# Performance work log

Hardware: AMD Instinct MI355X
Metric: run time of the kernel (lower is better)

Reference implementation:

```python
import jax, jax.numpy as jnp
import numpy as np

B, P, IN, OUT = 32, 128, 64, 32

def _logm(S):
    # symmetric PD matrix log via eigh: U diag(log w) U^T
    w, U = jnp.linalg.eigh(S)
    return jnp.einsum('...ij,...j,...kj->...ik', U, jnp.log(w), U)

def _expm(S):
    w, U = jnp.linalg.eigh(S)
    return jnp.einsum('...ij,...j,...kj->...ik', U, jnp.exp(w), U)

def setup_inputs() -> dict:
    key = jax.random.key(0)
    k1, k2, k3, k4 = jax.random.split(key, 4)
    # SPD input: A A^T / n + eps I
    A = jax.random.normal(k1, (B, P, IN, IN), dtype=jnp.float32)
    x = A @ jnp.swapaxes(A, -1, -2) / IN + 1e-3 * jnp.eye(IN, dtype=jnp.float32)
    scale = 1.0 / np.sqrt(IN)
    Wq = jax.random.normal(k2, (OUT, IN), dtype=jnp.float32) * scale
    Wk = jax.random.normal(k3, (OUT, IN), dtype=jnp.float32) * scale
    Wv = jax.random.normal(k4, (OUT, IN), dtype=jnp.float32) * scale
    return {"x": x, "Wq": Wq, "Wk": Wk, "Wv": Wv}

def reference(x, Wq, Wk, Wv):
    def bimap(W, S):  # W S W^T, keeps SPD
        return jnp.einsum('oi,bpij,kj->bpok', W, S, W)
    Q = bimap(Wq, x)   # (B,P,OUT,OUT)
    K = bimap(Wk, x)
    V = bimap(Wv, x)
    LQ, LK, LV = _logm(Q), _logm(K), _logm(V)
    # log-Euclidean squared distance d_ij = ||log Qi - log Kj||_F^2
    qq = jnp.sum(LQ * LQ, axis=(-2, -1))          # (B,P)
    kk = jnp.sum(LK * LK, axis=(-2, -1))          # (B,P)
    qk = jnp.einsum('bpij,bqij->bpq', LQ, LK)     # (B,P,P)
    energy = jnp.maximum(qq[:, :, None] + kk[:, None, :] - 2.0 * qk, 0.0)
    weights = 1.0 / (1.0 + jnp.log1p(energy))     # (B,Pq,Pk)
    prob = jax.nn.softmax(weights, axis=-2)       # softmax over query axis (dim=-2)
    prob = jnp.transpose(prob, (0, 2, 1))         # (B,P,P)
    # weighted Frechet (log-Euclidean) mean: exp(sum_j w_ij log V_j)
    mean_log = jnp.einsum('bij,bjkl->bikl', prob, LV)  # (B,P,OUT,OUT)
    return _expm(mean_log)
```

## Files before the change

kernel.cpp:

```cpp
#include <hip/hip_runtime.h>
#include <math.h>

#define NB   32
#define NP   128
#define NM   4096
#define NMAT3 12288

typedef float v2f __attribute__((ext_vector_type(2)));

#if defined(__has_builtin)
#if __has_builtin(__builtin_elementwise_fma)
#define V2FMA(x, y, z) __builtin_elementwise_fma((x), (y), (z))
#else
#define V2FMA(x, y, z) (v2f){fmaf((x).x, (y).x, (z).x), fmaf((x).y, (y).y, (z).y)}
#endif
#else
#define V2FMA(x, y, z) (v2f){fmaf((x).x, (y).x, (z).x), fmaf((x).y, (y).y, (z).y)}
#endif

__global__ __launch_bounds__(256) void bimap_kernel(
    const float* __restrict__ x, const float* __restrict__ Wq,
    const float* __restrict__ Wk, const float* __restrict__ Wv,
    float* __restrict__ qkv)
{
    __shared__ __align__(16) float S[64 * 64];
    __shared__ float Wl[32 * 65];
    __shared__ float T[32 * 65];
    const int tid = threadIdx.x;
    const int bp  = blockIdx.x;
    const float* xs = x + (size_t)bp * 4096;
#pragma unroll
    for (int k = 0; k < 4; ++k) {
        int idx = tid * 4 + k * 1024;
        *(float4*)&S[idx] = *(const float4*)&xs[idx];
    }
    const int o32 = tid & 31;
    const int grp = tid >> 5;
#pragma unroll 1
    for (int w = 0; w < 3; ++w) {
        const float* Wsrc = (w == 0) ? Wq : ((w == 1) ? Wk : Wv);
        __syncthreads();
#pragma unroll
        for (int k = 0; k < 8; ++k) {
            int f = tid + k * 256;
            Wl[(f >> 6) * 65 + (f & 63)] = Wsrc[f];
        }
        __syncthreads();
        {
            float acc[8];
#pragma unroll
            for (int jj = 0; jj < 8; ++jj) acc[jj] = 0.f;
            const int j0 = grp * 8;
#pragma unroll 4
            for (int i = 0; i < 64; ++i) {
                float wv = Wl[o32 * 65 + i];
                const float4 s0 = *(const float4*)&S[i * 64 + j0];
                const float4 s1 = *(const float4*)&S[i * 64 + j0 + 4];
                acc[0] = fmaf(wv, s0.x, acc[0]);
                acc[1] = fmaf(wv, s0.y, acc[1]);
                acc[2] = fmaf(wv, s0.z, acc[2]);
                acc[3] = fmaf(wv, s0.w, acc[3]);
                acc[4] = fmaf(wv, s1.x, acc[4]);
                acc[5] = fmaf(wv, s1.y, acc[5]);
                acc[6] = fmaf(wv, s1.z, acc[6]);
                acc[7] = fmaf(wv, s1.w, acc[7]);
            }
#pragma unroll
            for (int jj = 0; jj < 8; ++jj) T[o32 * 65 + j0 + jj] = acc[jj];
        }
        __syncthreads();
        {
            float oacc[4] = {0.f, 0.f, 0.f, 0.f};
            const int kcol = tid & 31;
            const int ob   = grp * 4;
#pragma unroll 4
            for (int j = 0; j < 64; ++j) {
                float wv = Wl[kcol * 65 + j];
#pragma unroll
                for (int cc = 0; cc < 4; ++cc)
                    oacc[cc] = fmaf(T[(ob + cc) * 65 + j], wv, oacc[cc]);
            }
            float* dst = qkv + ((size_t)w * NM + bp) * 1024;
#pragma unroll
            for (int cc = 0; cc < 4; ++cc)
                dst[(ob + cc) * 32 + kcol] = oacc[cc];
        }
    }
}

__device__ __forceinline__ float ror1(float x) {
    return __int_as_float(__builtin_amdgcn_mov_dpp(
        __float_as_int(x), 0x121, 0xf, 0xf, true));
}
__device__ __forceinline__ float ror15(float x) {
    return __int_as_float(__builtin_amdgcn_mov_dpp(
        __float_as_int(x), 0x12F, 0xf, 0xf, true));
}

__device__ __forceinline__ float dot16(const v2f (&x)[8], const v2f (&y)[8]) {
    v2f g0 = {0.f, 0.f}, g1 = {0.f, 0.f};
#pragma unroll
    for (int j = 0; j < 8; j += 2) {
        g0 = V2FMA(x[j], y[j], g0);
        g1 = V2FMA(x[j + 1], y[j + 1], g1);
    }
    v2f g = g0 + g1;
    return g.x + g.y;
}

__device__ __forceinline__ void jupdate(v2f (&a)[8], v2f (&b)[8],
                                        float& alA, float& alB,
                                        float gm, bool doRot) {
    const float zeta = (alB - alA) * __builtin_amdgcn_rcpf(2.0f * gm);
    float tt = copysignf(__builtin_amdgcn_rcpf(
        fabsf(zeta) + __builtin_amdgcn_sqrtf(fmaf(zeta, zeta, 1.0f))), zeta);
    float cc = __builtin_amdgcn_rsqf(fmaf(tt, tt, 1.0f));
    float sn = cc * tt;
    if (!doRot) { cc = 1.0f; sn = 0.0f; }
    const v2f c2 = {cc, cc}, sp = {sn, sn}, sm = {-sn, -sn};
#pragma unroll
    for (int j = 0; j < 8; ++j) {
        const v2f ao = a[j], bo = b[j];
        a[j] = V2FMA(c2, ao, sm * bo);
        b[j] = V2FMA(c2, bo, sp * ao);
    }
    const float cq = cc * cc, sq = sn * sn, cs2 = 2.0f * cc * sn * gm;
    const float nA = fmaf(cq, alA, fmaf(sq, alB, -cs2));
    const float nB = fmaf(sq, alA, fmaf(cq, alB, cs2));
    alA = nA; alB = nB;
}

template <int MODE>
__global__ __launch_bounds__(256) void eig_fn_kernel(
    const float* in, float* out, float* __restrict__ ssq, float shift)
{
    __shared__ __align__(16) float Uld[4][32 * 36];
    __shared__ __align__(16) float fld[4][32];
    const int tid  = threadIdx.x;
    const int wv   = tid >> 6;
    const int lane = tid & 63;
    const int idx  = lane & 15;
    const int h    = (lane >> 4) & 1;
    const int mw   = lane >> 5;
    const bool l14 = (idx == 14), l15 = (idx == 15);
    const int cA = idx * 2, cB = idx * 2 + 1;
    const int r0 = h * 16;
    const size_t m0 = (size_t)blockIdx.x * 8 + wv * 2;

    const float* src = in + (m0 + mw) * 1024;
    v2f a[8], b[8];
#pragma unroll
    for (int j = 0; j < 8; ++j) {
        const int rA = r0 + 2 * j, rB = rA + 1;
        float2 lo = *(const float2*)&src[rA * 32 + cA];
        float2 hi = *(const float2*)&src[rB * 32 + cA];
        v2f av = {lo.x, hi.x};
        v2f bv = {lo.y, hi.y};
        if (MODE == 1) {
            if (rA == cA) av.x += shift;
            if (rB == cA) av.y += shift;
            if (rA == cB) bv.x += shift;
            if (rB == cB) bv.y += shift;
        }
        a[j] = av; b[j] = bv;
    }

    for (int sweep = 0; sweep < 10; ++sweep) {
        float alA = dot16(a, a); alA += __shfl_xor(alA, 16);
        float alB = dot16(b, b); alB += __shfl_xor(alB, 16);
        bool bigrot = false;
        for (int r = 0; r < 31; ++r) {
            float gm = dot16(a, b);
            gm += __shfl_xor(gm, 16);
            const float t  = alA * alB;
            const float g2 = gm * gm;
            const bool doRot = g2 > 1e-10f * t;
            bigrot |= (g2 > 1e-7f * t);
            if (__any((int)doRot))
                jupdate(a, b, alA, alB, gm, doRot);
            {
                const float alAg = ror1(alA), alBg = ror15(alB), alAo = alA;
                alA = l15 ? alBg : alAg;
                alB = l15 ? alB : (l14 ? alAo : alBg);
            }
#pragma unroll
            for (int j = 0; j < 8; ++j) {
                const v2f ao = a[j], bo = b[j];
                v2f t2, an;
                t2.x = ror15(bo.x); t2.y = ror15(bo.y);
                an.x = ror1(ao.x);  an.y = ror1(ao.y);
                a[j] = l15 ? t2 : an;
                v2f bn = l14 ? ao : t2;
                b[j] = l15 ? bo : bn;
            }
        }
        if (!__any((int)bigrot)) break;
    }

    float s2A = dot16(a, a); s2A += __shfl_xor(s2A, 16);
    float s2B = dot16(b, b); s2B += __shfl_xor(s2B, 16);
    const float invA = __builtin_amdgcn_rsqf(fmaxf(s2A, 1e-30f));
    const float invB = __builtin_amdgcn_rsqf(fmaxf(s2B, 1e-30f));
    float fvA, fvB;
    if (MODE == 0) {
        fvA = 0.5f * logf(fmaxf(s2A, 1e-38f));
        fvB = 0.5f * logf(fmaxf(s2B, 1e-38f));
    } else {
        fvA = expf(__builtin_amdgcn_sqrtf(s2A) - shift);
        fvB = expf(__builtin_amdgcn_sqrtf(s2B) - shift);
    }

    if (MODE == 0) {
        float sq = fvA * fvA + fvB * fvB;
#pragma unroll
        for (int off = 1; off < 16; off <<= 1) sq += __shfl_xor(sq, off);
        if ((lane & 31) == 0) ssq[m0 + mw] = sq;
    }

    const int c  = lane & 31;
    const int hh = lane >> 5;
    float* Uw = &Uld[wv][0];
    float* fw = &fld[wv][0];
#pragma unroll 1
    for (int p = 0; p < 2; ++p) {
        __syncthreads();
        if (mw == p) {
#pragma unroll
            for (int j = 0; j < 8; ++j) {
                const int rA = r0 + 2 * j, rB = rA + 1;
                Uw[rA * 36 + cA] = a[j].x * invA;
                Uw[rB * 36 + cA] = a[j].y * invA;
                Uw[rA * 36 + cB] = b[j].x * invB;
                Uw[rB * 36 + cB] = b[j].y * invB;
            }
            if (h == 0) { fw[cA] = fvA; fw[cB] = fvB; }
        }
        __syncthreads();
        float rr[32];
        {
            const float4* urow = (const float4*)&Uw[c * 36];
            const float4* frow = (const float4*)&fw[0];
#pragma unroll
            for (int m4 = 0; m4 < 8; ++m4) {
                float4 u4 = urow[m4];
                float4 f4 = frow[m4];
                rr[m4 * 4 + 0] = u4.x * f4.x;
                rr[m4 * 4 + 1] = u4.y * f4.y;
                rr[m4 * 4 + 2] = u4.z * f4.z;
                rr[m4 * 4 + 3] = u4.w * f4.w;
            }
        }
        float* dst = out + (m0 + p) * 1024;
#pragma unroll
        for (int i = 0; i < 16; ++i) {
            const int row = hh * 16 + i;
            float acc = 0.f;
            const float4* urow = (const float4*)&Uw[row * 36];
#pragma unroll
            for (int m4 = 0; m4 < 8; ++m4) {
                float4 u4 = urow[m4];
                acc = fmaf(u4.x, rr[m4 * 4 + 0], acc);
                acc = fmaf(u4.y, rr[m4 * 4 + 1], acc);
                acc = fmaf(u4.z, rr[m4 * 4 + 2], acc);
                acc = fmaf(u4.w, rr[m4 * 4 + 3], acc);
            }
            dst[row * 32 + c] = acc;
        }
    }
}

__global__ __launch_bounds__(256) void qk_weights_kernel(
    const float* __restrict__ L, const float* __restrict__ ssq,
    float* __restrict__ wbuf)
{
    __shared__ float Aq[32 * 37];
    __shared__ float Bk[32 * 37];
    const int b  = blockIdx.z;
    const int q0 = blockIdx.y * 32;
    const int k0 = blockIdx.x * 32;
    const int tid = threadIdx.x;
    const int tx = tid & 15, ty = tid >> 4;
    const float* LQ = L + ((size_t)b * 128 + q0) * 1024;
    const float* LK = L + (size_t)NM * 1024 + ((size_t)b * 128 + k0) * 1024;
    const int lrow = tid >> 3;
    const int lm4  = (tid & 7) * 4;
    float acc00 = 0, acc01 = 0, acc10 = 0, acc11 = 0;
    for (int m0 = 0; m0 < 1024; m0 += 32) {
        __syncthreads();
        float4 va = *(const float4*)&LQ[(size_t)lrow * 1024 + m0 + lm4];
        float4 vb = *(const float4*)&LK[(size_t)lrow * 1024 + m0 + lm4];
        Aq[lrow * 37 + lm4 + 0] = va.x; Aq[lrow * 37 + lm4 + 1] = va.y;
        Aq[lrow * 37 + lm4 + 2] = va.z; Aq[lrow * 37 + lm4 + 3] = va.w;
        Bk[lrow * 37 + lm4 + 0] = vb.x; Bk[lrow * 37 + lm4 + 1] = vb.y;
        Bk[lrow * 37 + lm4 + 2] = vb.z; Bk[lrow * 37 + lm4 + 3] = vb.w;
        __syncthreads();
#pragma unroll
        for (int mm = 0; mm < 32; ++mm) {
            float a0 = Aq[(ty * 2 + 0) * 37 + mm];
            float a1 = Aq[(ty * 2 + 1) * 37 + mm];
            float b0 = Bk[(tx * 2 + 0) * 37 + mm];
            float b1 = Bk[(tx * 2 + 1) * 37 + mm];
            acc00 = fmaf(a0, b0, acc00); acc01 = fmaf(a0, b1, acc01);
            acc10 = fmaf(a1, b0, acc10); acc11 = fmaf(a1, b1, acc11);
        }
    }
    const float* qqp = ssq + (size_t)b * 128 + q0;
    const float* kkp = ssq + NM + (size_t)b * 128 + k0;
    const int q = ty * 2, k = tx * 2;
    float* wrow0 = wbuf + ((size_t)b * 128 + q0 + q) * 128 + k0 + k;
    float* wrow1 = wrow0 + 128;
    float e;
    e = fmaxf(qqp[q] + kkp[k] - 2.0f * acc00, 0.0f);
    wrow0[0] = 1.0f / (1.0f + log1pf(e));
    e = fmaxf(qqp[q] + kkp[k + 1] - 2.0f * acc01, 0.0f);
    wrow0[1] = 1.0f / (1.0f + log1pf(e));
    e = fmaxf(qqp[q + 1] + kkp[k] - 2.0f * acc10, 0.0f);
    wrow1[0] = 1.0f / (1.0f + log1pf(e));
    e = fmaxf(qqp[q + 1] + kkp[k + 1] - 2.0f * acc11, 0.0f);
    wrow1[1] = 1.0f / (1.0f + log1pf(e));
}

__global__ __launch_bounds__(256) void softmax_kernel(float* __restrict__ wbuf)
{
    __shared__ float crcp[128];
    const int t = threadIdx.x;
    float* wb = wbuf + (size_t)blockIdx.x * 16384;
    if (t < 128) {
        float ssum = 0.f;
        for (int q = 0; q < 128; ++q) ssum += expf(wb[q * 128 + t]);
        crcp[t] = 1.0f / ssum;
    }
    __syncthreads();
    for (int i = t; i < 16384; i += 256)
        wb[i] = expf(wb[i]) * crcp[i & 127];
}

__global__ __launch_bounds__(256) void meanlog_kernel(
    const float* __restrict__ soft, const float* __restrict__ LV,
    float* __restrict__ ML)
{
    __shared__ float Wt[32 * 129];
    __shared__ __align__(16) float Bl[32 * 260];
    const int b  = blockIdx.z;
    const int i0 = blockIdx.y * 32;
    const int c0 = blockIdx.x * 256;
    const int t  = threadIdx.x;
    const float* sp = soft + (size_t)b * 16384;
#pragma unroll
    for (int jb = 0; jb < 4; ++jb) {
        int j  = jb * 32 + (t >> 3);
        int i4 = (t & 7) * 4;
        float4 v = *(const float4*)&sp[(size_t)j * 128 + i0 + i4];
        Wt[(i4 + 0) * 129 + j] = v.x;
        Wt[(i4 + 1) * 129 + j] = v.y;
        Wt[(i4 + 2) * 129 + j] = v.z;
        Wt[(i4 + 3) * 129 + j] = v.w;
    }
    float acc[32];
#pragma unroll
    for (int i = 0; i < 32; ++i) acc[i] = 0.f;
    const float* lv = LV + (size_t)2 * NM * 1024 + (size_t)b * 128 * 1024 + c0;
    for (int j0 = 0; j0 < 128; j0 += 32) {
        __syncthreads();
#pragma unroll
        for (int jj8 = 0; jj8 < 8; ++jj8) {
            int j  = jj8 * 4 + (t >> 6);
            int c4 = (t & 63) * 4;
            *(float4*)&Bl[j * 260 + c4] =
                *(const float4*)&lv[(size_t)(j0 + j) * 1024 + c4];
        }
        __syncthreads();
#pragma unroll
        for (int jj = 0; jj < 32; ++jj) {
            float v = Bl[jj * 260 + t];
#pragma unroll
            for (int i = 0; i < 32; ++i)
                acc[i] = fmaf(Wt[i * 129 + j0 + jj], v, acc[i]);
        }
    }
    float* mp = ML + ((size_t)b * 128 + i0) * 1024 + c0;
#pragma unroll
    for (int i = 0; i < 32; ++i) mp[(size_t)i * 1024 + t] = acc[i];
}

extern "C" void kernel_launch(void* const* d_in, const int* in_sizes, int n_in,
                              void* d_out, int out_size, void* d_ws, size_t ws_size,
                              hipStream_t stream)
{
    const float* x  = (const float*)d_in[0];
    const float* Wq = (const float*)d_in[1];
    const float* Wk = (const float*)d_in[2];
    const float* Wv = (const float*)d_in[3];
    float* ws   = (float*)d_ws;
    float* qkv  = ws;
    float* ssqp = ws + (size_t)3 * NM * 1024;
    float* wbuf = ssqp + 16384;
    float* out  = (float*)d_out;

    bimap_kernel<<<NM, 256, 0, stream>>>(x, Wq, Wk, Wv, qkv);
    eig_fn_kernel<0><<<NMAT3 / 8, 256, 0, stream>>>(qkv, qkv, ssqp, 0.0f);
    qk_weights_kernel<<<dim3(4, 4, 32), 256, 0, stream>>>(qkv, ssqp, wbuf);
    softmax_kernel<<<32, 256, 0, stream>>>(wbuf);
    meanlog_kernel<<<dim3(4, 4, 32), 256, 0, stream>>>(wbuf, qkv, qkv);
    eig_fn_kernel<1><<<NM / 8, 256, 0, stream>>>(qkv, out, nullptr, 16.0f);
}
```

Baseline: 846.6 us.

## Replace eigendecomposition-based expm with scaling-and-squaring Taylor series

The final matrix exponential no longer goes through a Jacobi eigensolver. A new kernel scales each 32x32 matrix by 1/32, evaluates a degree-8 Taylor polynomial in Horner form with register-resident matrix products through LDS, then squares five times. This drops the iterative, data-dependent Jacobi sweeps in exchange for a fixed count of dense 32x32 matmuls. Accuracy now depends on the norm of the mean-log matrices staying small enough for the chosen scaling and degree.

```diff
diff --git a/kernel.cpp b/kernel.cpp
--- a/kernel.cpp
+++ b/kernel.cpp
@@ -8,15 +8,17 @@
 
 typedef float v2f __attribute__((ext_vector_type(2)));
 
+__device__ __forceinline__ v2f v2fma(v2f x, v2f y, v2f z) {
 #if defined(__has_builtin)
 #if __has_builtin(__builtin_elementwise_fma)
-#define V2FMA(x, y, z) __builtin_elementwise_fma((x), (y), (z))
+    return __builtin_elementwise_fma(x, y, z);
 #else
-#define V2FMA(x, y, z) (v2f){fmaf((x).x, (y).x, (z).x), fmaf((x).y, (y).y, (z).y)}
+    return (v2f){fmaf(x.x, y.x, z.x), fmaf(x.y, y.y, z.y)};
 #endif
 #else
-#define V2FMA(x, y, z) (v2f){fmaf((x).x, (y).x, (z).x), fmaf((x).y, (y).y, (z).y)}
+    return (v2f){fmaf(x.x, y.x, z.x), fmaf(x.y, y.y, z.y)};
 #endif
+}
 
 __global__ __launch_bounds__(256) void bimap_kernel(
     const float* __restrict__ x, const float* __restrict__ Wq,
@@ -101,8 +103,8 @@
     v2f g0 = {0.f, 0.f}, g1 = {0.f, 0.f};
 #pragma unroll
     for (int j = 0; j < 8; j += 2) {
-        g0 = V2FMA(x[j], y[j], g0);
-        g1 = V2FMA(x[j + 1], y[j + 1], g1);
+        g0 = v2fma(x[j], y[j], g0);
+        g1 = v2fma(x[j + 1], y[j + 1], g1);
     }
     v2f g = g0 + g1;
     return g.x + g.y;
@@ -121,8 +123,8 @@
 #pragma unroll
     for (int j = 0; j < 8; ++j) {
         const v2f ao = a[j], bo = b[j];
-        a[j] = V2FMA(c2, ao, sm * bo);
-        b[j] = V2FMA(c2, bo, sp * ao);
+        a[j] = v2fma(c2, ao, sm * bo);
+        b[j] = v2fma(c2, bo, sp * ao);
     }
     const float cq = cc * cc, sq = sn * sn, cs2 = 2.0f * cc * sn * gm;
     const float nA = fmaf(cq, alA, fmaf(sq, alB, -cs2));
@@ -130,9 +132,8 @@
     alA = nA; alB = nB;
 }
 
-template <int MODE>
-__global__ __launch_bounds__(256) void eig_fn_kernel(
-    const float* in, float* out, float* __restrict__ ssq, float shift)
+__global__ __launch_bounds__(256) void log_eig_kernel(
+    const float* in, float* out, float* __restrict__ ssq)
 {
     __shared__ __align__(16) float Uld[4][32 * 36];
     __shared__ __align__(16) float fld[4][32];
@@ -154,15 +155,8 @@
         const int rA = r0 + 2 * j, rB = rA + 1;
         float2 lo = *(const float2*)&src[rA * 32 + cA];
         float2 hi = *(const float2*)&src[rB * 32 + cA];
-        v2f av = {lo.x, hi.x};
-        v2f bv = {lo.y, hi.y};
-        if (MODE == 1) {
-            if (rA == cA) av.x += shift;
-            if (rB == cA) av.y += shift;
-            if (rA == cB) bv.x += shift;
-            if (rB == cB) bv.y += shift;
-        }
-        a[j] = av; b[j] = bv;
+        a[j] = (v2f){lo.x, hi.x};
+        b[j] = (v2f){lo.y, hi.y};
     }
 
     for (int sweep = 0; sweep < 10; ++sweep) {
@@ -201,16 +195,10 @@
     float s2B = dot16(b, b); s2B += __shfl_xor(s2B, 16);
     const float invA = __builtin_amdgcn_rsqf(fmaxf(s2A, 1e-30f));
     const float invB = __builtin_amdgcn_rsqf(fmaxf(s2B, 1e-30f));
-    float fvA, fvB;
-    if (MODE == 0) {
-        fvA = 0.5f * logf(fmaxf(s2A, 1e-38f));
-        fvB = 0.5f * logf(fmaxf(s2B, 1e-38f));
-    } else {
-        fvA = expf(__builtin_amdgcn_sqrtf(s2A) - shift);
-        fvB = expf(__builtin_amdgcn_sqrtf(s2B) - shift);
-    }
-
-    if (MODE == 0) {
+    const float fvA = 0.5f * logf(fmaxf(s2A, 1e-38f));
+    const float fvB = 0.5f * logf(fmaxf(s2B, 1e-38f));
+
+    {
         float sq = fvA * fvA + fvB * fvB;
 #pragma unroll
         for (int off = 1; off < 16; off <<= 1) sq += __shfl_xor(sq, off);
@@ -266,6 +254,102 @@
             }
             dst[row * 32 + c] = acc;
         }
+    }
+}
+
+__global__ __launch_bounds__(256) void expm_kernel(
+    const float* __restrict__ S, float* __restrict__ out)
+{
+    __shared__ __align__(16) float Mld[8][32 * 36];
+    const int tid  = threadIdx.x;
+    const int wv   = tid >> 6;
+    const int lane = tid & 63;
+    const int mw   = lane >> 5;
+    const int c    = lane & 31;
+    const int mi   = wv * 2 + mw;
+    const size_t midx = (size_t)blockIdx.x * 8 + mi;
+    float* Xl = &Mld[mi][0];
+
+    {
+        const float* sb = S + (size_t)blockIdx.x * 8192;
+#pragma unroll
+        for (int it = 0; it < 8; ++it) {
+            const int f   = tid * 4 + it * 1024;
+            const int mat = f >> 10;
+            const int r   = (f >> 5) & 31;
+            const int c0  = f & 31;
+            float4 g = *(const float4*)&sb[f];
+            g.x *= 0.03125f; g.y *= 0.03125f; g.z *= 0.03125f; g.w *= 0.03125f;
+            *(float4*)&Mld[mat][r * 36 + c0] = g;
+        }
+    }
+    __syncthreads();
+
+    v2f p[16];
+#pragma unroll
+    for (int t = 0; t < 16; ++t) {
+        float lo = Xl[(2 * t) * 36 + c] * 0.125f + ((2 * t) == c ? 1.f : 0.f);
+        float hi = Xl[(2 * t + 1) * 36 + c] * 0.125f + ((2 * t + 1) == c ? 1.f : 0.f);
+        p[t] = (v2f){lo, hi};
+    }
+
+#pragma unroll 1
+    for (int d = 7; d >= 1; --d) {
+        const float invd = __builtin_amdgcn_rcpf((float)d);
+        v2f np[16];
+#pragma unroll
+        for (int r = 0; r < 32; ++r) {
+            const float4* row = (const float4*)&Xl[r * 36];
+            v2f acc = {0.f, 0.f};
+#pragma unroll
+            for (int m4 = 0; m4 < 8; ++m4) {
+                float4 u = row[m4];
+                v2f u01 = {u.x, u.y};
+                v2f u23 = {u.z, u.w};
+                acc = v2fma(u01, p[2 * m4], acc);
+                acc = v2fma(u23, p[2 * m4 + 1], acc);
+            }
+            const float val = fmaf(acc.x + acc.y, invd, (r == c) ? 1.f : 0.f);
+            if (r & 1) np[r >> 1].y = val; else np[r >> 1].x = val;
+        }
+#pragma unroll
+        for (int t = 0; t < 16; ++t) p[t] = np[t];
+    }
+
+#pragma unroll 1
+    for (int t5 = 0; t5 < 5; ++t5) {
+        __syncthreads();
+#pragma unroll
+        for (int k = 0; k < 16; ++k) {
+            Xl[(2 * k) * 36 + c]     = p[k].x;
+            Xl[(2 * k + 1) * 36 + c] = p[k].y;
+        }
+        __syncthreads();
+        v2f np[16];
+#pragma unroll
+        for (int r = 0; r < 32; ++r) {
+            const float4* row = (const float4*)&Xl[r * 36];
+            v2f acc = {0.f, 0.f};
+#pragma unroll
+            for (int m4 = 0; m4 < 8; ++m4) {
+                float4 u = row[m4];
+                v2f u01 = {u.x, u.y};
+                v2f u23 = {u.z, u.w};
+                acc = v2fma(u01, p[2 * m4], acc);
+                acc = v2fma(u23, p[2 * m4 + 1], acc);
+            }
+            const float val = acc.x + acc.y;
+            if (r & 1) np[r >> 1].y = val; else np[r >> 1].x = val;
+        }
+#pragma unroll
+        for (int k = 0; k < 16; ++k) p[k] = np[k];
+    }
+
+    float* dst = out + midx * 1024;
+#pragma unroll
+    for (int k = 0; k < 16; ++k) {
+        dst[(2 * k) * 32 + c]     = p[k].x;
+        dst[(2 * k + 1) * 32 + c] = p[k].y;
     }
 }
 
@@ -398,9 +482,9 @@
     float* out  = (float*)d_out;
 
     bimap_kernel<<<NM, 256, 0, stream>>>(x, Wq, Wk, Wv, qkv);
-    eig_fn_kernel<0><<<NMAT3 / 8, 256, 0, stream>>>(qkv, qkv, ssqp, 0.0f);
+    log_eig_kernel<<<NMAT3 / 8, 256, 0, stream>>>(qkv, qkv, ssqp);
     qk_weights_kernel<<<dim3(4, 4, 32), 256, 0, stream>>>(qkv, ssqp, wbuf);
     softmax_kernel<<<32, 256, 0, stream>>>(wbuf);
     meanlog_kernel<<<dim3(4, 4, 32), 256, 0, stream>>>(wbuf, qkv, qkv);
-    eig_fn_kernel<1><<<NM / 8, 256, 0, stream>>>(qkv, out, nullptr, 16.0f);
-}
+    expm_kernel<<<NM / 8, 256, 0, stream>>>(qkv, out);
+}
```

Result: slower. 1.507 ms (+78.0%).
